# Kernel tuning notes

Measured on AMD Instinct MI355X. Metric: run time of the kernel, lower is better.

The kernel has to match this reference:

```python
import jax, jax.numpy as jnp
import numpy as np

CAL = {
 'x': (-0.0025095, 0.0022181),
 'onnxMatMul_166': (-0.22075387835502625, 0.208940327167511),
 'fc1MatMul': (-0.00291599917, 0.0017367251),
 'fc1bias': (-0.48688140511512756, 0.5176185369491577),
 'fc1Add': (-0.48778465390205383, 0.5181604027748108),
 'Wiz_1': (-0.43284985423088074, 0.46175122261047363),
 'Wir_1': (-0.34401071071624756, 0.29191476106643677),
 'Win_1': (-0.3236880302429199, 0.39607325196266174),
 'Whz_1': (-1.8417714834213257, 1.7173254489898682),
 'Whr_1': (-1.1574513912200928, 1.0300449132919312),
 'Whn_1': (-0.7756922245025635, 0.9530389308929443),
 'biz_1': (-0.5063393712043762, 0.36664387583732605),
 'bir_1': (-0.07920225709676743, 0.20611026883125305),
 'bin_1': (-0.5539973378181458, 0.17938342690467834),
 'bhz_1': (-0.5337516665458679, 0.4148772358894348),
 'bhr_1': (-0.07688436657190323, 0.14814253151416779),
 'bhn_1': (-0.7828555107116699, 0.9008108973503113),
 'Wiz_2': (-0.9102030992507935, 0.9408696889877319),
 'Wir_2': (-0.9560997486114502, 0.6683358550071716),
 'Win_2': (-0.4721935987472534, 0.48561596870422363),
 'Whz_2': (-1.2992678880691528, 1.2991048097610474),
 'Whr_2': (-0.8318714499473572, 1.1085889339447021),
 'Whn_2': (-0.955470085144043, 1.046797513961792),
 'biz_2': (-0.44805487990379333, 0.1560053527355194),
 'bir_2': (-0.08767592161893845, 0.11347303539514542),
 'bin_2': (-0.239909827709198, 0.12033259868621826),
 'bhz_2': (-0.43745461106300354, 0.12699371576309204),
 'bhr_2': (-0.09617264568805695, 0.07690174877643585),
 'bhn_2': (-0.17204178869724274, 0.19739042222499847),
 'onnxMatMul_207': (-1.3657219409942627, 1.158295750617981),
 'fc2bias': (-0.1750922054052353, 0.1385071724653244),
 'onnxMatMul_208': (-3.1666038036346436, 2.5026357173919678),
 'fc3bias': (-0.10188056528568268, 0.0899151861667633),
 'onnxMatMul_209': (-1.300571084022522, 1.928941249847412),
 'fc4bias': (-0.10699586570262909, 0.04597663879394531),
 'h1': (-0.002647488145157695, 0.0028339680284261703),
 'h2': (-0.0031016061548143625, 0.0030250486452132463),
 'gru1_a_': (-0.6389939785003662, 0.7715625762939453),
 'gru1_a': (-0.6046768426895142, 0.8871182203292847),
 'gru1_b_': (-0.004922409541904926, 0.004103424027562141),
 'gru1_b': (-0.07475128024816513, 0.14630259573459625),
 'gru1_c_': (-1.5660111904144287, 1.0454494953155518),
 'gru1_c': (-1.9779117107391357, 1.3700535297393799),
 'gru1_d_': (-0.008429044857621193, 0.006403823848813772),
 'gru1_d': (-0.5529640316963196, 0.41507571935653687),
 'gru1_e_': (-1.3637111186981201, 1.018247127532959),
 'gru1_e': (-1.8583884239196777, 1.1587692499160767),
 'gru1_f_': (-0.005411399528384209, 0.0061536869034171104),
 'gru1_f': (-0.7833794355392456, 0.8978855013847351),
 'gru1_r_': (-0.6226556301116943, 0.9800534844398499),
 'gru1_r': (0.3491777181625366, 0.7271188497543335),
 'gru1_z_': (-2.392332077026367, 1.7851293087005615),
 'gru1_z': (0.08375928550958633, 0.856329083442688),
 'gru1_n1': (-0.5516456365585327, 0.4556601643562317),
 'gru1_n2': (-2.4100341796875, 1.1423156261444092),
 'gru1_n': (-0.983996570110321, 0.8151924014091492),
 'gru1_hn1': (0.143670916557312, 0.9162406921386719),
 'gru1_hn2': (-0.9015777111053467, 0.45391541719436646),
 'gru1_hn3': (-0.0016954239690676332, 0.0016671211924403906),
 'rnn1GRU': (-0.9016271829605103, 0.4546271562576294),
 'gru2_a_': (-0.681461751461029, 0.9113116264343262),
 'gru2_a': (-0.7149235010147095, 0.908741295337677),
 'gru2_b_': (-0.005148397758603096, 0.011014967225492),
 'gru2_b': (-0.09436552226543427, 0.07623167335987091),
 'gru2_c_': (-1.2279887199401855, 1.1102137565612793),
 'gru2_c': (-1.6760436296463013, 1.200895071029663),
 'gru2_d_': (-0.008141756057739258, 0.00894666276872158),
 'gru2_d': (-0.43875735998153687, 0.1262134611606598),
 'gru2_e_': (-0.6732944250106812, 0.6314664483070374),
}
# calib entries for gru2 past 'e_' were truncated in the source; reuse gru1 ranges
for _k in ['e', 'f_', 'f', 'r_', 'r', 'z_', 'z', 'n1', 'n2', 'n', 'hn1', 'hn2', 'hn3']:
    CAL.setdefault('gru2_' + _k, CAL['gru1_' + _k])
CAL['rnn2GRU'] = CAL['rnn1GRU']


def fq(x, name):
    """Per-tensor unsigned 8-bit fake-quantize/dequantize (CalibrationParam S/Z)."""
    mn, mx = CAL[name]
    s = (mx - mn) / 255.0  # 2**8 - 1
    z = float(round(-mn / s))
    q = jnp.clip(jnp.round(x / s) + z, 0.0, 255.0)
    y = (q - z) * s
    # straight-through: forward value is exact fake-quant, identity gradient
    return x + jax.lax.stop_gradient(y - x)


def _gru_layer(xs, Wiz, Wir, Win, Whz, Whr, Whn, biz, bir, binn, bhz, bhr, bhn, L):
    p = 'gru%d' % L
    Wiz = fq(Wiz, 'Wiz_%d' % L); Wir = fq(Wir, 'Wir_%d' % L); Win = fq(Win, 'Win_%d' % L)
    Whz = fq(Whz, 'Whz_%d' % L); Whr = fq(Whr, 'Whr_%d' % L); Whn = fq(Whn, 'Whn_%d' % L)
    biz = fq(biz, 'biz_%d' % L); bir = fq(bir, 'bir_%d' % L); binn = fq(binn, 'bin_%d' % L)
    bhz = fq(bhz, 'bhz_%d' % L); bhr = fq(bhr, 'bhr_%d' % L); bhn = fq(bhn, 'bhn_%d' % L)
    # input projections batched over all timesteps (xs: [T,B,H] time-major)
    A = fq(fq(jnp.einsum('tbi,ih->tbh', xs, Wir), p + '_a_') + bir, p + '_a')
    C = fq(fq(jnp.einsum('tbi,ih->tbh', xs, Wiz), p + '_c_') + biz, p + '_c')
    E = fq(fq(jnp.einsum('tbi,ih->tbh', xs, Win), p + '_e_') + binn, p + '_e')
    h0 = fq(jnp.zeros((xs.shape[1], Whz.shape[0]), xs.dtype), 'h%d' % L)

    def step(h, ace):
        a, c, e = ace
        b = fq(fq(h @ Whr, p + '_b_') + bhr, p + '_b')
        r = fq(jax.nn.sigmoid(fq(a + b, p + '_r_')), p + '_r')
        d = fq(fq(h @ Whz, p + '_d_') + bhz, p + '_d')
        z = fq(jax.nn.sigmoid(fq(c + d, p + '_z_')), p + '_z')
        f = fq(fq(h @ Whn, p + '_f_') + bhn, p + '_f')
        n = fq(jnp.tanh(fq(e + fq(r * f, p + '_n1'), p + '_n2')), p + '_n')
        hn2 = fq(fq(1.0 - z, p + '_hn1') * n, p + '_hn2')
        hn3 = fq(z * h, p + '_hn3')
        h_new = fq(hn2 + hn3, 'rnn%dGRU' % L)
        return h_new, h_new

    _, hs = jax.lax.scan(step, h0, (A, C, E))
    return hs


def setup_inputs() -> dict:
    B, T, F, H, D = 64, 1000, 257, 400, 600
    ks = iter(jax.random.split(jax.random.key(0), 64))

    def u(shape, name):
        mn, mx = CAL[name]
        return jax.random.uniform(next(ks), shape, jnp.float32, mn, mx)

    inp = {}
    inp['x'] = jax.random.normal(next(ks), (B, T, F), jnp.float32) * 0.001
    inp['W_fc1'] = u((F, H), 'onnxMatMul_166')
    inp['b_fc1'] = u((H,), 'fc1bias')
    for L in (1, 2):
        for g in ('z', 'r', 'n'):
            inp['Wi%s%d' % (g, L)] = u((H, H), 'Wi%s_%d' % (g, L))
            inp['Wh%s%d' % (g, L)] = u((H, H), 'Wh%s_%d' % (g, L))
            inp['bi%s%d' % (g, L)] = u((H,), 'bi%s_%d' % (g, L))
            inp['bh%s%d' % (g, L)] = u((H,), 'bh%s_%d' % (g, L))
    inp['W_fc2'] = u((H, D), 'onnxMatMul_207'); inp['b_fc2'] = u((D,), 'fc2bias')
    inp['W_fc3'] = u((D, D), 'onnxMatMul_208'); inp['b_fc3'] = u((D,), 'fc3bias')
    inp['W_fc4'] = u((D, F), 'onnxMatMul_209'); inp['b_fc4'] = u((F,), 'fc4bias')
    return inp


def reference(x, W_fc1, b_fc1, Wiz1, Wir1, Win1, Whz1, Whr1, Whn1, biz1, bir1, bin1, bhz1, bhr1, bhn1, Wiz2, Wir2, Win2, Whz2, Whr2, Whn2, biz2, bir2, bin2, bhz2, bhr2, bhn2, W_fc2, b_fc2, W_fc3, b_fc3, W_fc4, b_fc4):
    xq = fq(x, 'x')
    t = fq(jnp.einsum('bti,ih->bth', xq, fq(W_fc1, 'onnxMatMul_166')), 'fc1MatMul')
    t = fq(t + fq(b_fc1, 'fc1bias'), 'fc1Add')
    xs = jnp.swapaxes(t, 0, 1)  # [T,B,400]
    h1 = _gru_layer(xs, Wiz1, Wir1, Win1, Whz1, Whr1, Whn1, biz1, bir1, bin1, bhz1, bhr1, bhn1, 1)
    h2 = _gru_layer(h1, Wiz2, Wir2, Win2, Whz2, Whr2, Whn2, biz2, bir2, bin2, bhz2, bhr2, bhn2, 2)
    y = jnp.swapaxes(h2, 0, 1)  # [B,T,400]
    y = jax.nn.relu(jnp.einsum('bth,hd->btd', y, fq(W_fc2, 'onnxMatMul_207')) + fq(b_fc2, 'fc2bias'))
    y = jax.nn.relu(jnp.einsum('btd,de->bte', y, fq(W_fc3, 'onnxMatMul_208')) + fq(b_fc3, 'fc3bias'))
    y = jax.nn.sigmoid(jnp.einsum('bte,ef->btf', y, fq(W_fc4, 'onnxMatMul_209')) + fq(b_fc4, 'fc4bias'))
    return y
```

## Files before the change

kernel.cpp:

```cpp
#include <hip/hip_runtime.h>
#include <math.h>

#define DEV static __device__ __forceinline__

typedef int v4i __attribute__((ext_vector_type(4)));
typedef float v4f __attribute__((ext_vector_type(4)));
typedef __bf16 bf16_t;
typedef __bf16 v8bf __attribute__((ext_vector_type(8)));

struct SZ { float s, z; };

constexpr double cfloor_(double v){ long long i=(long long)v; return ((double)i > v) ? (double)(i-1) : (double)i; }
constexpr double cround_(double v){
  double fl = cfloor_(v); double fr = v - fl;
  return (fr > 0.5) ? fl + 1.0 : (fr < 0.5 ? fl : ((((long long)fl) & 1LL) == 0 ? fl : fl + 1.0));
}
constexpr SZ mksz(double mn, double mx){
  double s = (mx - mn) / 255.0;
  double z = cround_(-mn / s);
  return SZ{ (float)s, (float)z };
}

constexpr SZ Zx     = mksz(-0.0025095, 0.0022181);
constexpr SZ ZW1    = mksz(-0.22075387835502625, 0.208940327167511);
constexpr SZ Zfc1mm = mksz(-0.00291599917, 0.0017367251);
constexpr SZ Zbfc1  = mksz(-0.48688140511512756, 0.5176185369491577);
constexpr SZ Zfc1add= mksz(-0.48778465390205383, 0.5181604027748108);
constexpr SZ ZWiz1 = mksz(-0.43284985423088074, 0.46175122261047363);
constexpr SZ ZWir1 = mksz(-0.34401071071624756, 0.29191476106643677);
constexpr SZ ZWin1 = mksz(-0.3236880302429199, 0.39607325196266174);
constexpr SZ ZWhz1 = mksz(-1.8417714834213257, 1.7173254489898682);
constexpr SZ ZWhr1 = mksz(-1.1574513912200928, 1.0300449132919312);
constexpr SZ ZWhn1 = mksz(-0.7756922245025635, 0.9530389308929443);
constexpr SZ Zbiz1 = mksz(-0.5063393712043762, 0.36664387583732605);
constexpr SZ Zbir1 = mksz(-0.07920225709676743, 0.20611026883125305);
constexpr SZ Zbin1 = mksz(-0.5539973378181458, 0.17938342690467834);
constexpr SZ Zbhz1 = mksz(-0.5337516665458679, 0.4148772358894348);
constexpr SZ Zbhr1 = mksz(-0.07688436657190323, 0.14814253151416779);
constexpr SZ Zbhn1 = mksz(-0.7828555107116699, 0.9008108973503113);
constexpr SZ ZWiz2 = mksz(-0.9102030992507935, 0.9408696889877319);
constexpr SZ ZWir2 = mksz(-0.9560997486114502, 0.6683358550071716);
constexpr SZ ZWin2 = mksz(-0.4721935987472534, 0.48561596870422363);
constexpr SZ ZWhz2 = mksz(-1.2992678880691528, 1.2991048097610474);
constexpr SZ ZWhr2 = mksz(-0.8318714499473572, 1.1085889339447021);
constexpr SZ ZWhn2 = mksz(-0.955470085144043, 1.046797513961792);
constexpr SZ Zbiz2 = mksz(-0.44805487990379333, 0.1560053527355194);
constexpr SZ Zbir2 = mksz(-0.08767592161893845, 0.11347303539514542);
constexpr SZ Zbin2 = mksz(-0.239909827709198, 0.12033259868621826);
constexpr SZ Zbhz2 = mksz(-0.43745461106300354, 0.12699371576309204);
constexpr SZ Zbhr2 = mksz(-0.09617264568805695, 0.07690174877643585);
constexpr SZ Zbhn2 = mksz(-0.17204178869724274, 0.19739042222499847);
constexpr SZ ZWfc2 = mksz(-1.3657219409942627, 1.158295750617981);
constexpr SZ Zbfc2 = mksz(-0.1750922054052353, 0.1385071724653244);
constexpr SZ ZWfc3 = mksz(-3.1666038036346436, 2.5026357173919678);
constexpr SZ Zbfc3 = mksz(-0.10188056528568268, 0.0899151861667633);
constexpr SZ ZWfc4 = mksz(-1.300571084022522, 1.928941249847412);
constexpr SZ Zbfc4 = mksz(-0.10699586570262909, 0.04597663879394531);
constexpr SZ Za_1 = mksz(-0.6389939785003662, 0.7715625762939453);
constexpr SZ Za1  = mksz(-0.6046768426895142, 0.8871182203292847);
constexpr SZ Zb_1 = mksz(-0.004922409541904926, 0.004103424027562141);
constexpr SZ Zb1  = mksz(-0.07475128024816513, 0.14630259573459625);
constexpr SZ Zc_1 = mksz(-1.5660111904144287, 1.0454494953155518);
constexpr SZ Zc1  = mksz(-1.9779117107391357, 1.3700535297393799);
constexpr SZ Zd_1 = mksz(-0.008429044857621193, 0.006403823848813772);
constexpr SZ Zd1  = mksz(-0.5529640316963196, 0.41507571935653687);
constexpr SZ Ze_1 = mksz(-1.3637111186981201, 1.018247127532959);
constexpr SZ Ze1  = mksz(-1.8583884239196777, 1.1587692499160767);
constexpr SZ Zf_1 = mksz(-0.005411399528384209, 0.0061536869034171104);
constexpr SZ Zf1  = mksz(-0.7833794355392456, 0.8978855013847351);
constexpr SZ Zr_1 = mksz(-0.6226556301116943, 0.9800534844398499);
constexpr SZ Zr1  = mksz(0.3491777181625366, 0.7271188497543335);
constexpr SZ Zz_1 = mksz(-2.392332077026367, 1.7851293087005615);
constexpr SZ Zz1  = mksz(0.08375928550958633, 0.856329083442688);
constexpr SZ Zn11 = mksz(-0.5516456365585327, 0.4556601643562317);
constexpr SZ Zn21 = mksz(-2.4100341796875, 1.1423156261444092);
constexpr SZ Zn1  = mksz(-0.983996570110321, 0.8151924014091492);
constexpr SZ Zhn11= mksz(0.143670916557312, 0.9162406921386719);
constexpr SZ Zhn21= mksz(-0.9015777111053467, 0.45391541719436646);
constexpr SZ Zhn31= mksz(-0.0016954239690676332, 0.0016671211924403906);
constexpr SZ Zrnn = mksz(-0.9016271829605103, 0.4546271562576294);
constexpr SZ Za_2 = mksz(-0.681461751461029, 0.9113116264343262);
constexpr SZ Za2  = mksz(-0.7149235010147095, 0.908741295337677);
constexpr SZ Zb_2 = mksz(-0.005148397758603096, 0.011014967225492);
constexpr SZ Zb2g = mksz(-0.09436552226543427, 0.07623167335987091);
constexpr SZ Zc_2 = mksz(-1.2279887199401855, 1.1102137565612793);
constexpr SZ Zc2  = mksz(-1.6760436296463013, 1.200895071029663);
constexpr SZ Zd_2 = mksz(-0.008141756057739258, 0.00894666276872158);
constexpr SZ Zd2  = mksz(-0.43875735998153687, 0.1262134611606598);
constexpr SZ Ze_2 = mksz(-0.6732944250106812, 0.6314664483070374);

struct RecP {
  SZ wr, wz, wn;
  SZ a, c, e;
  SZ b1, b2, d1, d2, f1, f2;
  SZ r1, r2, z1, z2;
  SZ n1, n2, n3;
  SZ hn1, hn2, hn3, rnn;
};
constexpr RecP PL1 = { ZWhr1, ZWhz1, ZWhn1, Za1, Zc1, Ze1, Zb_1, Zb1, Zd_1, Zd1, Zf_1, Zf1,
                       Zr_1, Zr1, Zz_1, Zz1, Zn11, Zn21, Zn1, Zhn11, Zhn21, Zhn31, Zrnn };
constexpr RecP PL2 = { ZWhr2, ZWhz2, ZWhn2, Za2, Zc2, Ze1, Zb_2, Zb2g, Zd_2, Zd2, Zf_1, Zf1,
                       Zr_1, Zr1, Zz_1, Zz1, Zn11, Zn21, Zn1, Zhn11, Zhn21, Zhn31, Zrnn };

DEV float fq_(float x, float s, float z){
  float q = rintf(x / s) + z;
  q = fminf(fmaxf(q, 0.f), 255.f);
  return (q - z) * s;
}
DEV float sigm_(float v){ return 1.f / (1.f + expf(-v)); }

DEV unsigned udot4_(unsigned a, unsigned b, unsigned c){
#if defined(__has_builtin) && __has_builtin(__builtin_amdgcn_udot4)
  return __builtin_amdgcn_udot4(a, b, c, false);
#else
  return c + (a & 255u) * (b & 255u) + ((a >> 8) & 255u) * ((b >> 8) & 255u)
           + ((a >> 16) & 255u) * ((b >> 16) & 255u) + (a >> 24) * (b >> 24);
#endif
}

struct BJob { const float* src; float* dst; int n; float s; float z; };
struct BJobs { BJob j[16]; };
__global__ __launch_bounds__(256) void kbias(BJobs jobs){
  BJob J = jobs.j[blockIdx.x];
  for (int i = threadIdx.x; i < J.n; i += 256) J.dst[i] = fq_(J.src[i], J.s, J.z);
}

struct W6 { const float* W[6]; float s[6]; float z[6]; };
__global__ __launch_bounds__(256) void kwhc6(W6 jb, unsigned char* __restrict__ dst){
  int i = blockIdx.x * 256 + threadIdx.x;
  if (i < 960000) {
    int m = i / 160000, r = i - m * 160000;
    int j = r / 400, k = r - j * 400;
    float q = rintf(jb.W[m][k * 400 + j] / jb.s[m]) + jb.z[m];
    q = fminf(fmaxf(q, 0.f), 255.f);
    dst[i] = (unsigned char)q;
  }
}
__global__ __launch_bounds__(256) void kcolsum(const unsigned char* __restrict__ WhC, int* __restrict__ cs){
  int i = blockIdx.x * 256 + threadIdx.x;
  if (i < 2400) {
    const unsigned char* p = WhC + (size_t)i * 400;
    int s = 0;
    for (int k = 0; k < 400; ++k) s += p[k];
    cs[i] = s;
  }
}
__global__ __launch_bounds__(256) void kwic6(W6 jb, signed char* __restrict__ WiT, int* __restrict__ cs){
  for (int idx = blockIdx.x * 256 + threadIdx.x; idx < 960000; idx += gridDim.x * 256) {
    int m = idx / 160000, r = idx - m * 160000;
    int k = r / 400, n = r - k * 400;
    float q = rintf(jb.W[m][r] / jb.s[m]) + jb.z[m];
    q = fminf(fmaxf(q, 0.f), 255.f);
    int qi = (int)q;
    WiT[(size_t)m * 185600 + (size_t)n * 464 + k] = (signed char)(qi ^ 0x80);
    atomicAdd(&cs[m * 400 + n], qi - 128);
  }
  for (int idx = blockIdx.x * 256 + threadIdx.x; idx < 153600; idx += gridDim.x * 256) {
    int m = idx / 25600, r = idx - m * 25600;
    int n = r / 64, p = r - n * 64;
    WiT[(size_t)m * 185600 + (size_t)n * 464 + 400 + p] = 0;
  }
}
__global__ __launch_bounds__(256) void kwic(const float* __restrict__ W, signed char* __restrict__ Bt,
                                            int* __restrict__ cs, float s, float z, int K, int N){
  int total1 = K * N, total2 = (464 - K) * N;
  for (int idx = blockIdx.x * 256 + threadIdx.x; idx < total1; idx += gridDim.x * 256) {
    int k = idx / N, n = idx - k * N;
    float q = rintf(W[idx] / s) + z;
    q = fminf(fmaxf(q, 0.f), 255.f);
    int qi = (int)q;
    Bt[(size_t)n * 464 + k] = (signed char)(qi ^ 0x80);
    atomicAdd(&cs[n], qi - 128);
  }
  for (int idx = blockIdx.x * 256 + threadIdx.x; idx < total2; idx += gridDim.x * 256) {
    int n = idx / (464 - K), k = K + (idx - n * (464 - K));
    Bt[(size_t)n * 464 + k] = 0;
  }
}
__global__ __launch_bounds__(256) void kwbf(const float* __restrict__ W, bf16_t* __restrict__ Bt,
                                            float s, float z, int K, int N){
  int total1 = K * N, total2 = (608 - K) * N;
  for (int idx = blockIdx.x * 256 + threadIdx.x; idx < total1; idx += gridDim.x * 256) {
    int k = idx / N, n = idx - k * N;
    float q = rintf(W[idx] / s) + z;
    q = fminf(fmaxf(q, 0.f), 255.f);
    Bt[(size_t)n * 608 + k] = (bf16_t)(q - z);
  }
  for (int idx = blockIdx.x * 256 + threadIdx.x; idx < total2; idx += gridDim.x * 256) {
    int n = idx / (608 - K), k = K + (idx - n * (608 - K));
    Bt[(size_t)n * 608 + k] = (bf16_t)0.f;
  }
}
__global__ __launch_bounds__(256) void kxq(const float* __restrict__ x, unsigned char* __restrict__ xcq,
                                           float s, float z){
  int idx = blockIdx.x * 256 + threadIdx.x;
  if (idx < 64000 * 464) {
    int row = idx / 464, c = idx - row * 464;
    unsigned char code = 128;
    if (c < 257) {
      int bb = row & 63, tt = row >> 6;
      float q = rintf(x[((size_t)bb * 1000 + tt) * 257 + c] / s) + z;
      q = fminf(fmaxf(q, 0.f), 255.f);
      code = (unsigned char)q;
    }
    xcq[idx] = code;
  }
}
__global__ __launch_bounds__(256) void krsum(const unsigned char* __restrict__ A, int* __restrict__ rs,
                                             int w4){
  int r = blockIdx.x * 256 + threadIdx.x;
  const unsigned* p = (const unsigned*)(A + (size_t)r * (w4 * 16));
  unsigned s = 0;
  for (int i = 0; i < w4 * 4; ++i) s = udot4_(p[i], 0x01010101u, s);
  rs[r] = (int)s - 128 * 4 * (w4 * 4);
}
__global__ __launch_bounds__(256) void kinit2(unsigned long long* __restrict__ hp1,
                                              unsigned long long* __restrict__ hp2, unsigned code){
  int i = blockIdx.x * 256 + threadIdx.x;
  if (i < 25600) {
    unsigned long long w = (unsigned long long)(code * 0x01010101u);
    hp1[i] = w; hp2[i] = w;
  }
}

__global__ __launch_bounds__(256) void gemm_i8(
    const unsigned char* __restrict__ Au8, int strideA, int aw4,
    const int* __restrict__ rowsum,
    const signed char* __restrict__ Bt, const int* __restrict__ colsum,
    const float* __restrict__ bias,
    unsigned char* __restrict__ outU8, float* __restrict__ outF,
    int N, int nb, int outStride, int epMode,
    int czw, int cza, int cconst, float ss,
    float e1S, float e1Z, float e2S, float e2Z)
{
  __shared__ __align__(16) signed char Asl[64 * 464];
  __shared__ __align__(16) signed char Bsl[80 * 464];
  const int tid = threadIdx.x;
  const int bm = blockIdx.x / nb;
  const int bn = blockIdx.x - bm * nb;
  const int m0 = bm * 64;
  const int n0 = bn * 80;
  for (int i = tid; i < 80 * 29; i += 256) {
    int r = i / 29, c = i - r * 29;
    uint4 v;
    if (n0 + r < N) v = *(const uint4*)(Bt + (size_t)(n0 + r) * 464 + c * 16);
    else { v.x = 0u; v.y = 0u; v.z = 0u; v.w = 0u; }
    *(uint4*)(Bsl + (size_t)r * 464 + c * 16) = v;
  }
  for (int i = tid; i < 64 * 29; i += 256) {
    int r = i / 29, c = i - r * 29;
    uint4 v;
    if (c < aw4) {
      v = *(const uint4*)(Au8 + (size_t)(m0 + r) * strideA + c * 16);
      v.x ^= 0x80808080u; v.y ^= 0x80808080u; v.z ^= 0x80808080u; v.w ^= 0x80808080u;
    } else { v.x = 0u; v.y = 0u; v.z = 0u; v.w = 0u; }
    *(uint4*)(Asl + (size_t)r * 464 + c * 16) = v;
  }
  __syncthreads();
  const int wv = tid >> 6, ln = tid & 63;
  const int lr = ln & 15;
  const int lk = ln >> 4;
  v4i acc[5];
#pragma unroll
  for (int j = 0; j < 5; ++j) { acc[j][0] = 0; acc[j][1] = 0; acc[j][2] = 0; acc[j][3] = 0; }
#pragma unroll
  for (int kc = 0; kc < 7; ++kc) {
    int kb = kc * 64 + lk * 16;
    v4i a = *(const v4i*)(Asl + (size_t)(wv * 16 + lr) * 464 + kb);
#pragma unroll
    for (int j = 0; j < 5; ++j) {
      v4i b = *(const v4i*)(Bsl + (size_t)(j * 16 + lr) * 464 + kb);
      acc[j] = __builtin_amdgcn_mfma_i32_16x16x64_i8(a, b, acc[j], 0, 0, 0);
    }
  }
#pragma unroll
  for (int reg = 0; reg < 4; ++reg) {
    int row = m0 + wv * 16 + lk * 4 + reg;
    int RA = rowsum[row];
#pragma unroll
    for (int j = 0; j < 5; ++j) {
      int col = n0 + j * 16 + lr;
      if (col >= N) continue;
      int I = acc[j][reg] + czw * RA + cza * colsum[col] + cconst;
      float v = (float)I * ss;
      if (epMode == 0) {
        v = fq_(v, e1S, e1Z) + bias[col];
        float q = rintf(v / e2S) + e2Z;
        q = fminf(fmaxf(q, 0.f), 255.f);
        outU8[(size_t)row * outStride + col] = (unsigned char)q;
      } else {
        v += bias[col];
        v = fmaxf(v, 0.f);
        outF[(size_t)row * outStride + col] = v;
      }
    }
  }
}

__global__ __launch_bounds__(512) void gemm_bf(
    const float* __restrict__ A, const bf16_t* __restrict__ Bt,
    const float* __restrict__ bias, float* __restrict__ outF,
    int N, int nb, int epMode, int rowOff, float sc)
{
  __shared__ __align__(16) bf16_t Bs[128 * 616];
  const int tid = threadIdx.x;
  const int bm = blockIdx.x / nb;
  const int bn = blockIdx.x - bm * nb;
  const int m0 = bm * 128;
  const int n0 = bn * 128;
  for (int i = tid; i < 128 * 76; i += 512) {
    int r = i / 76, c = i - r * 76;
    uint4 v; v.x = 0u; v.y = 0u; v.z = 0u; v.w = 0u;
    if (n0 + r < N) v = *(const uint4*)((const char*)(Bt + (size_t)(n0 + r) * 608) + c * 16);
    *(uint4*)((char*)(Bs + (size_t)r * 616) + c * 16) = v;
  }
  __syncthreads();
  const int wv = tid >> 6, ln = tid & 63;
  const int lr = ln & 15, quad = ln >> 4;
  const float* arp = A + (size_t)(m0 + wv * 16 + lr) * 600;
  v4f acc[8];
#pragma unroll
  for (int j = 0; j < 8; ++j) { acc[j][0] = 0.f; acc[j][1] = 0.f; acc[j][2] = 0.f; acc[j][3] = 0.f; }
  for (int kc = 0; kc < 19; ++kc) {
    int kb = kc * 32 + quad * 8;
    float af[8];
    if (kc == 18 && quad == 3) {
#pragma unroll
      for (int j = 0; j < 8; ++j) af[j] = 0.f;
    } else {
      *(float4*)&af[0] = *(const float4*)(arp + kb);
      *(float4*)&af[4] = *(const float4*)(arp + kb + 4);
    }
    v8bf ah, al;
#pragma unroll
    for (int j = 0; j < 8; ++j) {
      float xx = af[j];
      bf16_t h = (bf16_t)xx;
      ah[j] = h;
      al[j] = (bf16_t)(xx - (float)h);
    }
#pragma unroll
    for (int nf = 0; nf < 8; ++nf) {
      v8bf bfrag = *(const v8bf*)(Bs + (size_t)(nf * 16 + lr) * 616 + kc * 32 + quad * 8);
      acc[nf] = __builtin_amdgcn_mfma_f32_16x16x32_bf16(ah, bfrag, acc[nf], 0, 0, 0);
      acc[nf] = __builtin_amdgcn_mfma_f32_16x16x32_bf16(al, bfrag, acc[nf], 0, 0, 0);
    }
  }
#pragma unroll
  for (int nf = 0; nf < 8; ++nf) {
    int col = n0 + nf * 16 + lr;
    if (col >= N) continue;
    float bcol = bias[col];
#pragma unroll
    for (int reg = 0; reg < 4; ++reg) {
      int row = m0 + wv * 16 + quad * 4 + reg;
      float v = acc[nf][reg] * sc + bcol;
      if (epMode == 2) {
        v = fmaxf(v, 0.f);
        outF[(size_t)row * N + col] = v;
      } else {
        v = sigm_(v);
        int rg = rowOff + row;
        int tt = rg >> 6, bb = rg & 63;
        outF[((size_t)bb * 1000 + tt) * 257 + col] = v;
      }
    }
  }
}

__global__ __launch_bounds__(512)
__attribute__((amdgpu_num_vgpr(160)))
void gru_rec2b(
    const unsigned char* __restrict__ WhC, const int* __restrict__ colsum,
    const unsigned char* __restrict__ Aq, const unsigned char* __restrict__ Cq,
    const unsigned char* __restrict__ Eq,
    const float* __restrict__ bhr, const float* __restrict__ bhz, const float* __restrict__ bhn,
    unsigned char* __restrict__ hs, unsigned long long* __restrict__ hpub, RecP P)
{
  __shared__ __align__(16) unsigned Wl[352 * 28];
  __shared__ __align__(16) unsigned hq[2][4 * 28];
  __shared__ int dots_i[600];
  __shared__ unsigned acew[2][150];
  __shared__ int ic_l[600];
  __shared__ float bias_l[600];
  __shared__ int HqS_s;
  __shared__ int flag;

  const int tid = threadIdx.x;
  const int sl = blockIdx.x >> 6;
  const int b  = blockIdx.x & 63;
  const unsigned* Wu = (const unsigned*)WhC;

  unsigned wq[4][25];
#pragma unroll
  for (int s = 0; s < 4; ++s) {
    int q = tid + 512 * s;
    int ld = q >> 2, p = q & 3;
    int g = (ld >= 400) ? 2 : (ld >= 200 ? 1 : 0);
    int col = g * 400 + sl * 200 + (ld - g * 200);
    const unsigned* src = Wu + col * 100 + p * 25;
#pragma unroll
    for (int w = 0; w < 25; ++w) wq[s][w] = src[w];
  }
  if (tid < 352) {
    int q = 2048 + tid;
    int ld = q >> 2, p = q & 3;
    int g = (ld >= 400) ? 2 : (ld >= 200 ? 1 : 0);
    int col = g * 400 + sl * 200 + (ld - g * 200);
    const unsigned* src = Wu + col * 100 + p * 25;
    for (int w = 0; w < 25; ++w) Wl[tid * 28 + w] = src[w];
  }
  const int zh = (int)P.rnn.z;
  for (int ld = tid; ld < 600; ld += 512) {
    int g = (ld >= 400) ? 2 : (ld >= 200 ? 1 : 0);
    int jl = ld - g * 200;
    int col = g * 400 + sl * 200 + jl;
    int zw = (g == 0) ? (int)P.wr.z : (g == 1) ? (int)P.wz.z : (int)P.wn.z;
    ic_l[ld] = -zh * colsum[col] + 400 * zh * zw;
    bias_l[ld] = ((g == 0) ? bhr : (g == 1) ? bhz : bhn)[sl * 200 + jl];
  }
  const unsigned code0 = (unsigned)fminf(fmaxf(P.rnn.z, 0.f), 255.f);
  for (int i = tid; i < 100; i += 512)
    hq[0][(i / 25) * 28 + (i % 25)] = code0 * 0x01010101u;
  if (tid == 0) flag = -1;
  const unsigned char* psrc = nullptr;
  int poff = 0;
  if (tid < 150) {
    int g = tid / 50, w = tid - g * 50;
    psrc = (g == 0) ? Aq : (g == 1) ? Cq : Eq;
    poff = (sl * 50 + w) * 4;
    acew[0][tid] = *(const unsigned*)(psrc + (size_t)b * 400 + poff);
  }
  __syncthreads();

  const int part = tid & 3;
  const int grp = tid >> 2;
  const int zwr = (int)P.wr.z, zwz = (int)P.wz.z, zwn = (int)P.wn.z;
  const float swr = P.wr.s * P.rnn.s, swz = P.wz.s * P.rnn.s, swn = P.wn.s * P.rnn.s;
  unsigned long long* pubBase = hpub + (size_t)sl * 12800 + (size_t)b * 50;
  const unsigned long long* polBase = hpub + (size_t)(1 - sl) * 12800 + (size_t)b * 50;

  unsigned hcode = code0;
  unsigned pf = 0;

  for (int t = 0; t < 1000; ++t) {
    if (tid < 150) {
      int tn = (t + 1 < 1000) ? (t + 1) : 999;
      pf = *(const unsigned*)(psrc + ((size_t)tn * 64 + b) * 400 + poff);
    }
    if (tid >= 448) {
      int lane = tid - 448;
      unsigned pay = 0;
      if (lane < 50) {
        const unsigned long long* src = polBase + (size_t)(t & 3) * 3200 + lane;
        unsigned long long w64;
        while ((unsigned)((w64 = __hip_atomic_load(src, __ATOMIC_RELAXED, __HIP_MEMORY_SCOPE_AGENT)) >> 32)
               != (unsigned)t) { }
        pay = (unsigned)w64;
        int wd = (1 - sl) * 50 + lane;
        hq[t & 1][(wd / 25) * 28 + (wd % 25)] = pay;
      }
      if (lane == 0)
        __hip_atomic_store(&flag, t, __ATOMIC_RELEASE, __HIP_MEMORY_SCOPE_WORKGROUP);
      unsigned ssum = 0;
      if (lane < 50) {
        ssum = udot4_(pay, 0x01010101u, 0u);
        int wdo = sl * 50 + lane;
        unsigned own = hq[t & 1][(wdo / 25) * 28 + (wdo % 25)];
        ssum = udot4_(own, 0x01010101u, ssum);
      }
#pragma unroll
      for (int off = 32; off; off >>= 1) ssum += __shfl_down(ssum, off);
      if (lane == 0) HqS_s = (int)ssum;
    } else {
      while (__hip_atomic_load(&flag, __ATOMIC_ACQUIRE, __HIP_MEMORY_SCOPE_WORKGROUP) < t)
        __builtin_amdgcn_s_sleep(1);
    }
    const unsigned* hb = &hq[t & 1][part * 28];
    const unsigned* wl = &Wl[tid * 28];
    unsigned a0 = 0, a1 = 0, a2 = 0, a3 = 0, a4 = 0;
#pragma unroll
    for (int c = 0; c < 6; ++c) {
      uint4 h4 = *(const uint4*)(hb + 4 * c);
      a0 = udot4_(wq[0][4*c+0], h4.x, a0);
      a0 = udot4_(wq[0][4*c+1], h4.y, a0);
      a0 = udot4_(wq[0][4*c+2], h4.z, a0);
      a0 = udot4_(wq[0][4*c+3], h4.w, a0);
      a1 = udot4_(wq[1][4*c+0], h4.x, a1);
      a1 = udot4_(wq[1][4*c+1], h4.y, a1);
      a1 = udot4_(wq[1][4*c+2], h4.z, a1);
      a1 = udot4_(wq[1][4*c+3], h4.w, a1);
      a2 = udot4_(wq[2][4*c+0], h4.x, a2);
      a2 = udot4_(wq[2][4*c+1], h4.y, a2);
      a2 = udot4_(wq[2][4*c+2], h4.z, a2);
      a2 = udot4_(wq[2][4*c+3], h4.w, a2);
      a3 = udot4_(wq[3][4*c+0], h4.x, a3);
      a3 = udot4_(wq[3][4*c+1], h4.y, a3);
      a3 = udot4_(wq[3][4*c+2], h4.z, a3);
      a3 = udot4_(wq[3][4*c+3], h4.w, a3);
      if (tid < 352) {
        uint4 w4 = *(const uint4*)(wl + 4 * c);
        a4 = udot4_(w4.x, h4.x, a4);
        a4 = udot4_(w4.y, h4.y, a4);
        a4 = udot4_(w4.z, h4.z, a4);
        a4 = udot4_(w4.w, h4.w, a4);
      }
    }
    {
      unsigned hl = hb[24];
      a0 = udot4_(wq[0][24], hl, a0);
      a1 = udot4_(wq[1][24], hl, a1);
      a2 = udot4_(wq[2][24], hl, a2);
      a3 = udot4_(wq[3][24], hl, a3);
      if (tid < 352) a4 = udot4_(wl[24], hl, a4);
    }
    a0 += __shfl_xor(a0, 1); a0 += __shfl_xor(a0, 2);
    a1 += __shfl_xor(a1, 1); a1 += __shfl_xor(a1, 2);
    a2 += __shfl_xor(a2, 1); a2 += __shfl_xor(a2, 2);
    a3 += __shfl_xor(a3, 1); a3 += __shfl_xor(a3, 2);
    a4 += __shfl_xor(a4, 1); a4 += __shfl_xor(a4, 2);
    {
      int v = (part == 0) ? (int)a0 : (part == 1) ? (int)a1 : (part == 2) ? (int)a2 : (int)a3;
      dots_i[grp + 128 * part] = v;
      if (part == 0 && tid < 352) dots_i[512 + grp] = (int)a4;
    }
    __syncthreads();

    if (tid < 150) acew[(t + 1) & 1][tid] = pf;
    if (tid < 200) {
      const int j = tid;
      const unsigned char* ab = (const unsigned char*)&acew[t & 1][0];
      float av = ((float)ab[j]       - P.a.z) * P.a.s;
      float cv = ((float)ab[200 + j] - P.c.z) * P.c.s;
      float ev = ((float)ab[400 + j] - P.e.z) * P.e.s;
      int hqs = HqS_s;
      int Ib = dots_i[j]       - zwr * hqs + ic_l[j];
      int Id = dots_i[200 + j] - zwz * hqs + ic_l[200 + j];
      int If = dots_i[400 + j] - zwn * hqs + ic_l[400 + j];
      float bb = fq_((float)Ib * swr, P.b1.s, P.b1.z) + bias_l[j];
      bb = fq_(bb, P.b2.s, P.b2.z);
      float dd = fq_((float)Id * swz, P.d1.s, P.d1.z) + bias_l[200 + j];
      dd = fq_(dd, P.d2.s, P.d2.z);
      float ff = fq_((float)If * swn, P.f1.s, P.f1.z) + bias_l[400 + j];
      ff = fq_(ff, P.f2.s, P.f2.z);
      float r  = fq_(sigm_(fq_(av + bb, P.r1.s, P.r1.z)), P.r2.s, P.r2.z);
      float zz = fq_(sigm_(fq_(cv + dd, P.z1.s, P.z1.z)), P.z2.s, P.z2.z);
      float nn = fq_(tanhf(fq_(ev + fq_(r * ff, P.n1.s, P.n1.z), P.n2.s, P.n2.z)), P.n3.s, P.n3.z);
      float hold = ((float)hcode - P.rnn.z) * P.rnn.s;
      float hn2v = fq_(fq_(1.f - zz, P.hn1.s, P.hn1.z) * nn, P.hn2.s, P.hn2.z);
      float hn3v = fq_(zz * hold, P.hn3.s, P.hn3.z);
      float hnew = hn2v + hn3v;
      float qv = rintf(hnew / P.rnn.s) + P.rnn.z;
      qv = fminf(fmaxf(qv, 0.f), 255.f);
      unsigned code = (unsigned)qv;
      hcode = code;
      unsigned c1 = __shfl_down(code, 1);
      unsigned c2 = __shfl_down(code, 2);
      unsigned c3 = __shfl_down(code, 3);
      if ((j & 3) == 0) {
        unsigned packed = code | (c1 << 8) | (c2 << 16) | (c3 << 24);
        int wrd = j >> 2;
        int wd = sl * 50 + wrd;
        hq[(t + 1) & 1][(wd / 25) * 28 + (wd % 25)] = packed;
        *(unsigned*)(hs + ((size_t)t * 64 + b) * 400 + (wd << 2)) = packed;
        unsigned long long out64 = ((unsigned long long)(unsigned)(t + 1) << 32) | packed;
        __hip_atomic_store(pubBase + (size_t)((t + 1) & 3) * 3200 + wrd, out64,
                           __ATOMIC_RELAXED, __HIP_MEMORY_SCOPE_AGENT);
      }
    }
    __syncthreads();
  }
}

extern "C" void kernel_launch(void* const* d_in, const int* in_sizes, int n_in,
                              void* d_out, int out_size, void* d_ws, size_t ws_size,
                              hipStream_t stream)
{
  const float* x    = (const float*)d_in[0];
  const float* Wfc1 = (const float*)d_in[1];
  const float* bfc1 = (const float*)d_in[2];
  const float* Wiz1 = (const float*)d_in[3];  const float* Whz1 = (const float*)d_in[4];
  const float* biz1 = (const float*)d_in[5];  const float* bhz1 = (const float*)d_in[6];
  const float* Wir1 = (const float*)d_in[7];  const float* Whr1 = (const float*)d_in[8];
  const float* bir1 = (const float*)d_in[9];  const float* bhr1 = (const float*)d_in[10];
  const float* Win1 = (const float*)d_in[11]; const float* Whn1 = (const float*)d_in[12];
  const float* bin1 = (const float*)d_in[13]; const float* bhn1 = (const float*)d_in[14];
  const float* Wiz2 = (const float*)d_in[15]; const float* Whz2 = (const float*)d_in[16];
  const float* biz2 = (const float*)d_in[17]; const float* bhz2 = (const float*)d_in[18];
  const float* Wir2 = (const float*)d_in[19]; const float* Whr2 = (const float*)d_in[20];
  const float* bir2 = (const float*)d_in[21]; const float* bhr2 = (const float*)d_in[22];
  const float* Win2 = (const float*)d_in[23]; const float* Whn2 = (const float*)d_in[24];
  const float* bin2 = (const float*)d_in[25]; const float* bhn2 = (const float*)d_in[26];
  const float* Wfc2 = (const float*)d_in[27]; const float* bfc2 = (const float*)d_in[28];
  const float* Wfc3 = (const float*)d_in[29]; const float* bfc3 = (const float*)d_in[30];
  const float* Wfc4 = (const float*)d_in[31]; const float* bfc4 = (const float*)d_in[32];
  float* out = (float*)d_out;

  char* wp = (char*)d_ws;
  auto alloc = [&](size_t bytes) -> void* {
    void* p = (void*)wp;
    wp += (bytes + 255) & ~(size_t)255;
    return p;
  };
  float* b1q = (float*)alloc(400 * 4);
  float* biq = (float*)alloc(2400 * 4);
  float* bhq = (float*)alloc(2400 * 4);
  float* b2q = (float*)alloc(600 * 4);
  float* b3q = (float*)alloc(600 * 4);
  float* b4q = (float*)alloc(257 * 4);
  unsigned char* WhC = (unsigned char*)alloc(960000);
  int* colsum = (int*)alloc(2400 * 4);
  signed char* WiT = (signed char*)alloc(7 * 400 * 464);
  signed char* Bt2 = (signed char*)alloc(600 * 464);
  bf16_t* Bt3 = (bf16_t*)alloc(600 * 608 * 2);
  bf16_t* Bt4 = (bf16_t*)alloc(257 * 608 * 2);
  int* cwi = (int*)alloc((7 * 400 + 600) * 4);
  int* rsX1 = (int*)alloc(64000 * 4);
  int* rsX  = (int*)alloc(64000 * 4);
  int* rsH  = (int*)alloc(64000 * 4);
  int* rsH2 = (int*)alloc(64000 * 4);
  unsigned char* xsq = (unsigned char*)alloc(25600000);
  unsigned char* Aq  = (unsigned char*)alloc(25600000);
  unsigned char* Cq  = (unsigned char*)alloc(25600000);
  unsigned char* Eq  = (unsigned char*)alloc(25600000);
  unsigned char* hs1 = (unsigned char*)alloc(25600000);
  unsigned char* hs2 = (unsigned char*)alloc(25600000);
  unsigned long long* hpub1 = (unsigned long long*)alloc(25600 * 8);
  unsigned long long* hpub2 = (unsigned long long*)alloc(25600 * 8);
  float* y2c = (float*)Aq;
  float* y3c = (float*)(Aq + 38400000);
  unsigned char* xcq = hs1;

  BJobs bj;
  bj.j[0]  = { bfc1, b1q,        400, Zbfc1.s, Zbfc1.z };
  bj.j[1]  = { bir1, biq + 0,    400, Zbir1.s, Zbir1.z };
  bj.j[2]  = { biz1, biq + 400,  400, Zbiz1.s, Zbiz1.z };
  bj.j[3]  = { bin1, biq + 800,  400, Zbin1.s, Zbin1.z };
  bj.j[4]  = { bir2, biq + 1200, 400, Zbir2.s, Zbir2.z };
  bj.j[5]  = { biz2, biq + 1600, 400, Zbiz2.s, Zbiz2.z };
  bj.j[6]  = { bin2, biq + 2000, 400, Zbin2.s, Zbin2.z };
  bj.j[7]  = { bhr1, bhq + 0,    400, Zbhr1.s, Zbhr1.z };
  bj.j[8]  = { bhz1, bhq + 400,  400, Zbhz1.s, Zbhz1.z };
  bj.j[9]  = { bhn1, bhq + 800,  400, Zbhn1.s, Zbhn1.z };
  bj.j[10] = { bhr2, bhq + 1200, 400, Zbhr2.s, Zbhr2.z };
  bj.j[11] = { bhz2, bhq + 1600, 400, Zbhz2.s, Zbhz2.z };
  bj.j[12] = { bhn2, bhq + 2000, 400, Zbhn2.s, Zbhn2.z };
  bj.j[13] = { bfc2, b2q,        600, Zbfc2.s, Zbfc2.z };
  bj.j[14] = { bfc3, b3q,        600, Zbfc3.s, Zbfc3.z };
  bj.j[15] = { bfc4, b4q,        257, Zbfc4.s, Zbfc4.z };
  kbias<<<dim3(16), dim3(256), 0, stream>>>(bj);

  W6 wh = { { Whr1, Whz1, Whn1, Whr2, Whz2, Whn2 },
            { ZWhr1.s, ZWhz1.s, ZWhn1.s, ZWhr2.s, ZWhz2.s, ZWhn2.s },
            { ZWhr1.z, ZWhz1.z, ZWhn1.z, ZWhr2.z, ZWhz2.z, ZWhn2.z } };
  kwhc6<<<dim3(3750), dim3(256), 0, stream>>>(wh, WhC);
  kcolsum<<<dim3(10), dim3(256), 0, stream>>>(WhC, colsum);
  unsigned code0 = (unsigned)(Zrnn.z < 0.f ? 0.f : (Zrnn.z > 255.f ? 255.f : Zrnn.z));
  kinit2<<<dim3(100), dim3(256), 0, stream>>>(hpub1, hpub2, code0);

  hipMemsetAsync(cwi, 0, (7 * 400 + 600) * 4, stream);
  W6 wi = { { Wir1, Wiz1, Win1, Wir2, Wiz2, Win2 },
            { ZWir1.s, ZWiz1.s, ZWin1.s, ZWir2.s, ZWiz2.s, ZWin2.s },
            { ZWir1.z, ZWiz1.z, ZWin1.z, ZWir2.z, ZWiz2.z, ZWin2.z } };
  kwic6<<<dim3(625), dim3(256), 0, stream>>>(wi, WiT, cwi);
  kwic<<<dim3(625), dim3(256), 0, stream>>>(Wfc1, WiT + (size_t)6 * 185600, cwi + 2400, ZW1.s, ZW1.z, 257, 400);
  kwic<<<dim3(625), dim3(256), 0, stream>>>(Wfc2, Bt2, cwi + 2800, ZWfc2.s, ZWfc2.z, 400, 600);
  kwbf<<<dim3(625), dim3(256), 0, stream>>>(Wfc3, Bt3, ZWfc3.s, ZWfc3.z, 600, 600);
  kwbf<<<dim3(625), dim3(256), 0, stream>>>(Wfc4, Bt4, ZWfc4.s, ZWfc4.z, 600, 257);

  auto gi8 = [&](const unsigned char* A, int strideA, int aw4, const int* rs,
                 const signed char* Bt, const int* cs, const float* bias,
                 unsigned char* oU8, float* oF, int M, int N, int outStride, int epMode,
                 SZ a, SZ w, int Kreal, float ss, SZ e1, SZ e2) {
    int czw = 128 - (int)w.z, cza = 128 - (int)a.z;
    int cconst = Kreal * cza * czw;
    int nb = (N + 79) / 80;
    gemm_i8<<<dim3((M / 64) * nb), dim3(256), 0, stream>>>(
        A, strideA, aw4, rs, Bt, cs, bias, oU8, oF, N, nb, outStride, epMode,
        czw, cza, cconst, ss, e1.s, e1.z, e2.s, e2.z);
  };

  kxq<<<dim3((64000 * 464 + 255) / 256), dim3(256), 0, stream>>>(x, xcq, Zx.s, Zx.z);
  krsum<<<dim3(250), dim3(256), 0, stream>>>(xcq, rsX1, 29);
  gi8(xcq, 464, 29, rsX1, WiT + (size_t)6 * 185600, cwi + 2400, b1q,
      xsq, nullptr, 64000, 400, 400, 0, Zx, ZW1, 257, Zx.s * ZW1.s, Zfc1mm, Zfc1add);

  krsum<<<dim3(250), dim3(256), 0, stream>>>(xsq, rsX, 25);
  gi8(xsq, 400, 25, rsX, WiT + (size_t)0 * 185600, cwi + 0,    biq + 0,   Aq, nullptr,
      64000, 400, 400, 0, Zfc1add, ZWir1, 400, Zfc1add.s * ZWir1.s, Za_1, Za1);
  gi8(xsq, 400, 25, rsX, WiT + (size_t)1 * 185600, cwi + 400,  biq + 400, Cq, nullptr,
      64000, 400, 400, 0, Zfc1add, ZWiz1, 400, Zfc1add.s * ZWiz1.s, Zc_1, Zc1);
  gi8(xsq, 400, 25, rsX, WiT + (size_t)2 * 185600, cwi + 800,  biq + 800, Eq, nullptr,
      64000, 400, 400, 0, Zfc1add, ZWin1, 400, Zfc1add.s * ZWin1.s, Ze_1, Ze1);
  gru_rec2b<<<dim3(128), dim3(512), 0, stream>>>(WhC, colsum, Aq, Cq, Eq,
                                                 bhq + 0, bhq + 400, bhq + 800,
                                                 hs1, hpub1, PL1);
  krsum<<<dim3(250), dim3(256), 0, stream>>>(hs1, rsH, 25);
  gi8(hs1, 400, 25, rsH, WiT + (size_t)3 * 185600, cwi + 1200, biq + 1200, Aq, nullptr,
      64000, 400, 400, 0, Zrnn, ZWir2, 400, Zrnn.s * ZWir2.s, Za_2, Za2);
  gi8(hs1, 400, 25, rsH, WiT + (size_t)4 * 185600, cwi + 1600, biq + 1600, Cq, nullptr,
      64000, 400, 400, 0, Zrnn, ZWiz2, 400, Zrnn.s * ZWiz2.s, Zc_2, Zc2);
  gi8(hs1, 400, 25, rsH, WiT + (size_t)5 * 185600, cwi + 2000, biq + 2000, Eq, nullptr,
      64000, 400, 400, 0, Zrnn, ZWin2, 400, Zrnn.s * ZWin2.s, Ze_2, Ze1);
  gru_rec2b<<<dim3(128), dim3(512), 0, stream>>>(WhC + 480000, colsum + 1200, Aq, Cq, Eq,
                                                 bhq + 1200, bhq + 1600, bhq + 2000,
                                                 hs2, hpub2, PL2);
  krsum<<<dim3(250), dim3(256), 0, stream>>>(hs2, rsH2, 25);
  for (int rc = 0; rc < 4; ++rc) {
    const unsigned char* a2 = hs2 + (size_t)rc * 16000 * 400;
    gi8(a2, 400, 25, rsH2 + rc * 16000, Bt2, cwi + 2800, b2q, nullptr, y2c,
        16000, 600, 600, 2, Zrnn, ZWfc2, 400, Zrnn.s * ZWfc2.s, Zrnn, Zrnn);
    gemm_bf<<<dim3(125 * 5), dim3(512), 0, stream>>>(y2c, Bt3, b3q, y3c, 600, 5, 2, 0, ZWfc3.s);
    gemm_bf<<<dim3(125 * 3), dim3(512), 0, stream>>>(y3c, Bt4, b4q, out, 257, 3, 3, rc * 16000, ZWfc4.s);
  }
  (void)in_sizes; (void)n_in; (void)out_size; (void)ws_size;
}
```

Measured before the change: 6.850 ms.

## Split GRU recurrence across four workgroups per batch row instead of two

Each batch row's recurrent GRU step is now spread over four cooperating workgroups (256 blocks), each owning 100 hidden units, instead of two owning 200. The hidden-state exchange through the global publish buffer changes to an all-to-all among four slices, and each thread holds half as many weight registers. The VGPR cap and the s_sleep in the flag spin-wait are removed. The aim is to shorten the per-step serial dot-product and gate work, at the cost of more cross-block polling traffic and synchronisation per timestep.

```diff
diff --git a/kernel.cpp b/kernel.cpp
--- a/kernel.cpp
+++ b/kernel.cpp
@@ -368,21 +368,19 @@
   }
 }
 
-__global__ __launch_bounds__(512)
-__attribute__((amdgpu_num_vgpr(160)))
-void gru_rec2b(
+__global__ __launch_bounds__(512) void gru_rec4b(
     const unsigned char* __restrict__ WhC, const int* __restrict__ colsum,
     const unsigned char* __restrict__ Aq, const unsigned char* __restrict__ Cq,
     const unsigned char* __restrict__ Eq,
     const float* __restrict__ bhr, const float* __restrict__ bhz, const float* __restrict__ bhn,
     unsigned char* __restrict__ hs, unsigned long long* __restrict__ hpub, RecP P)
 {
-  __shared__ __align__(16) unsigned Wl[352 * 28];
+  __shared__ __align__(16) unsigned Wl[176 * 28];
   __shared__ __align__(16) unsigned hq[2][4 * 28];
-  __shared__ int dots_i[600];
-  __shared__ unsigned acew[2][150];
-  __shared__ int ic_l[600];
-  __shared__ float bias_l[600];
+  __shared__ int dots_i[300];
+  __shared__ unsigned acew[2][75];
+  __shared__ int ic_l[300];
+  __shared__ float bias_l[300];
   __shared__ int HqS_s;
   __shared__ int flag;
 
@@ -391,33 +389,33 @@
   const int b  = blockIdx.x & 63;
   const unsigned* Wu = (const unsigned*)WhC;
 
-  unsigned wq[4][25];
-#pragma unroll
-  for (int s = 0; s < 4; ++s) {
+  unsigned wq[2][25];
+#pragma unroll
+  for (int s = 0; s < 2; ++s) {
     int q = tid + 512 * s;
     int ld = q >> 2, p = q & 3;
-    int g = (ld >= 400) ? 2 : (ld >= 200 ? 1 : 0);
-    int col = g * 400 + sl * 200 + (ld - g * 200);
+    int g = ld / 100, jl = ld - g * 100;
+    int col = g * 400 + sl * 100 + jl;
     const unsigned* src = Wu + col * 100 + p * 25;
 #pragma unroll
     for (int w = 0; w < 25; ++w) wq[s][w] = src[w];
   }
-  if (tid < 352) {
-    int q = 2048 + tid;
+  if (tid < 176) {
+    int q = 1024 + tid;
     int ld = q >> 2, p = q & 3;
-    int g = (ld >= 400) ? 2 : (ld >= 200 ? 1 : 0);
-    int col = g * 400 + sl * 200 + (ld - g * 200);
+    int g = ld / 100, jl = ld - g * 100;
+    int col = g * 400 + sl * 100 + jl;
     const unsigned* src = Wu + col * 100 + p * 25;
     for (int w = 0; w < 25; ++w) Wl[tid * 28 + w] = src[w];
   }
   const int zh = (int)P.rnn.z;
-  for (int ld = tid; ld < 600; ld += 512) {
-    int g = (ld >= 400) ? 2 : (ld >= 200 ? 1 : 0);
-    int jl = ld - g * 200;
-    int col = g * 400 + sl * 200 + jl;
+  if (tid < 300) {
+    int ld = tid;
+    int g = ld / 100, jl = ld - g * 100;
+    int col = g * 400 + sl * 100 + jl;
     int zw = (g == 0) ? (int)P.wr.z : (g == 1) ? (int)P.wz.z : (int)P.wn.z;
     ic_l[ld] = -zh * colsum[col] + 400 * zh * zw;
-    bias_l[ld] = ((g == 0) ? bhr : (g == 1) ? bhz : bhn)[sl * 200 + jl];
+    bias_l[ld] = ((g == 0) ? bhr : (g == 1) ? bhz : bhn)[sl * 100 + jl];
   }
   const unsigned code0 = (unsigned)fminf(fmaxf(P.rnn.z, 0.f), 255.f);
   for (int i = tid; i < 100; i += 512)
@@ -425,10 +423,10 @@
   if (tid == 0) flag = -1;
   const unsigned char* psrc = nullptr;
   int poff = 0;
-  if (tid < 150) {
-    int g = tid / 50, w = tid - g * 50;
+  if (tid < 75) {
+    int g = tid / 25, w = tid - g * 25;
     psrc = (g == 0) ? Aq : (g == 1) ? Cq : Eq;
-    poff = (sl * 50 + w) * 4;
+    poff = (sl * 25 + w) * 4;
     acew[0][tid] = *(const unsigned*)(psrc + (size_t)b * 400 + poff);
   }
   __syncthreads();
@@ -437,48 +435,54 @@
   const int grp = tid >> 2;
   const int zwr = (int)P.wr.z, zwz = (int)P.wz.z, zwn = (int)P.wn.z;
   const float swr = P.wr.s * P.rnn.s, swz = P.wz.s * P.rnn.s, swn = P.wn.s * P.rnn.s;
-  unsigned long long* pubBase = hpub + (size_t)sl * 12800 + (size_t)b * 50;
-  const unsigned long long* polBase = hpub + (size_t)(1 - sl) * 12800 + (size_t)b * 50;
 
   unsigned hcode = code0;
   unsigned pf = 0;
 
   for (int t = 0; t < 1000; ++t) {
-    if (tid < 150) {
+    if (tid < 75) {
       int tn = (t + 1 < 1000) ? (t + 1) : 999;
       pf = *(const unsigned*)(psrc + ((size_t)tn * 64 + b) * 400 + poff);
     }
     if (tid >= 448) {
       int lane = tid - 448;
-      unsigned pay = 0;
-      if (lane < 50) {
-        const unsigned long long* src = polBase + (size_t)(t & 3) * 3200 + lane;
+      const unsigned long long* base = hpub + ((size_t)(t & 3) * 64 + b) * 100;
+      unsigned pay0, pay1 = 0;
+      {
+        int o = lane / 25, p = lane - o * 25;
+        int so = (sl + o + 1) & 3;
+        const unsigned long long* src = base + so * 25 + p;
         unsigned long long w64;
         while ((unsigned)((w64 = __hip_atomic_load(src, __ATOMIC_RELAXED, __HIP_MEMORY_SCOPE_AGENT)) >> 32)
                != (unsigned)t) { }
-        pay = (unsigned)w64;
-        int wd = (1 - sl) * 50 + lane;
-        hq[t & 1][(wd / 25) * 28 + (wd % 25)] = pay;
+        pay0 = (unsigned)w64;
+        hq[t & 1][so * 28 + p] = pay0;
+      }
+      if (lane < 11) {
+        int w1 = 64 + lane;
+        int o = w1 / 25, p = w1 - o * 25;
+        int so = (sl + o + 1) & 3;
+        const unsigned long long* src = base + so * 25 + p;
+        unsigned long long w64;
+        while ((unsigned)((w64 = __hip_atomic_load(src, __ATOMIC_RELAXED, __HIP_MEMORY_SCOPE_AGENT)) >> 32)
+               != (unsigned)t) { }
+        pay1 = (unsigned)w64;
+        hq[t & 1][so * 28 + p] = pay1;
       }
       if (lane == 0)
         __hip_atomic_store(&flag, t, __ATOMIC_RELEASE, __HIP_MEMORY_SCOPE_WORKGROUP);
-      unsigned ssum = 0;
-      if (lane < 50) {
-        ssum = udot4_(pay, 0x01010101u, 0u);
-        int wdo = sl * 50 + lane;
-        unsigned own = hq[t & 1][(wdo / 25) * 28 + (wdo % 25)];
-        ssum = udot4_(own, 0x01010101u, ssum);
-      }
-#pragma unroll
-      for (int off = 32; off; off >>= 1) ssum += __shfl_down(ssum, off);
+      unsigned ssum = udot4_(pay0, 0x01010101u, 0u);
+      if (lane < 11) ssum = udot4_(pay1, 0x01010101u, ssum);
+      if (lane < 25) ssum = udot4_(hq[t & 1][sl * 28 + lane], 0x01010101u, ssum);
+#pragma unroll
+      for (int off = 32; off; off >>= 1) ssum += __shfl_down(ssum, off, 64);
       if (lane == 0) HqS_s = (int)ssum;
     } else {
-      while (__hip_atomic_load(&flag, __ATOMIC_ACQUIRE, __HIP_MEMORY_SCOPE_WORKGROUP) < t)
-        __builtin_amdgcn_s_sleep(1);
+      while (__hip_atomic_load(&flag, __ATOMIC_ACQUIRE, __HIP_MEMORY_SCOPE_WORKGROUP) < t) { }
     }
     const unsigned* hb = &hq[t & 1][part * 28];
     const unsigned* wl = &Wl[tid * 28];
-    unsigned a0 = 0, a1 = 0, a2 = 0, a3 = 0, a4 = 0;
+    unsigned a0 = 0, a1 = 0, a2 = 0;
 #pragma unroll
     for (int c = 0; c < 6; ++c) {
       uint4 h4 = *(const uint4*)(hb + 4 * c);
@@ -490,58 +494,44 @@
       a1 = udot4_(wq[1][4*c+1], h4.y, a1);
       a1 = udot4_(wq[1][4*c+2], h4.z, a1);
       a1 = udot4_(wq[1][4*c+3], h4.w, a1);
-      a2 = udot4_(wq[2][4*c+0], h4.x, a2);
-      a2 = udot4_(wq[2][4*c+1], h4.y, a2);
-      a2 = udot4_(wq[2][4*c+2], h4.z, a2);
-      a2 = udot4_(wq[2][4*c+3], h4.w, a2);
-      a3 = udot4_(wq[3][4*c+0], h4.x, a3);
-      a3 = udot4_(wq[3][4*c+1], h4.y, a3);
-      a3 = udot4_(wq[3][4*c+2], h4.z, a3);
-      a3 = udot4_(wq[3][4*c+3], h4.w, a3);
-      if (tid < 352) {
+      if (tid < 176) {
         uint4 w4 = *(const uint4*)(wl + 4 * c);
-        a4 = udot4_(w4.x, h4.x, a4);
-        a4 = udot4_(w4.y, h4.y, a4);
-        a4 = udot4_(w4.z, h4.z, a4);
-        a4 = udot4_(w4.w, h4.w, a4);
+        a2 = udot4_(w4.x, h4.x, a2);
+        a2 = udot4_(w4.y, h4.y, a2);
+        a2 = udot4_(w4.z, h4.z, a2);
+        a2 = udot4_(w4.w, h4.w, a2);
       }
     }
     {
       unsigned hl = hb[24];
       a0 = udot4_(wq[0][24], hl, a0);
       a1 = udot4_(wq[1][24], hl, a1);
-      a2 = udot4_(wq[2][24], hl, a2);
-      a3 = udot4_(wq[3][24], hl, a3);
-      if (tid < 352) a4 = udot4_(wl[24], hl, a4);
+      if (tid < 176) a2 = udot4_(wl[24], hl, a2);
     }
     a0 += __shfl_xor(a0, 1); a0 += __shfl_xor(a0, 2);
     a1 += __shfl_xor(a1, 1); a1 += __shfl_xor(a1, 2);
     a2 += __shfl_xor(a2, 1); a2 += __shfl_xor(a2, 2);
-    a3 += __shfl_xor(a3, 1); a3 += __shfl_xor(a3, 2);
-    a4 += __shfl_xor(a4, 1); a4 += __shfl_xor(a4, 2);
-    {
-      int v = (part == 0) ? (int)a0 : (part == 1) ? (int)a1 : (part == 2) ? (int)a2 : (int)a3;
-      dots_i[grp + 128 * part] = v;
-      if (part == 0 && tid < 352) dots_i[512 + grp] = (int)a4;
-    }
+    if (part == 0)      dots_i[grp]       = (int)a0;
+    else if (part == 1) dots_i[128 + grp] = (int)a1;
+    else if (part == 2) { if (grp < 44) dots_i[256 + grp] = (int)a2; }
     __syncthreads();
 
-    if (tid < 150) acew[(t + 1) & 1][tid] = pf;
-    if (tid < 200) {
+    if (tid < 75) acew[(t + 1) & 1][tid] = pf;
+    if (tid < 100) {
       const int j = tid;
       const unsigned char* ab = (const unsigned char*)&acew[t & 1][0];
       float av = ((float)ab[j]       - P.a.z) * P.a.s;
-      float cv = ((float)ab[200 + j] - P.c.z) * P.c.s;
-      float ev = ((float)ab[400 + j] - P.e.z) * P.e.s;
+      float cv = ((float)ab[100 + j] - P.c.z) * P.c.s;
+      float ev = ((float)ab[200 + j] - P.e.z) * P.e.s;
       int hqs = HqS_s;
       int Ib = dots_i[j]       - zwr * hqs + ic_l[j];
-      int Id = dots_i[200 + j] - zwz * hqs + ic_l[200 + j];
-      int If = dots_i[400 + j] - zwn * hqs + ic_l[400 + j];
+      int Id = dots_i[100 + j] - zwz * hqs + ic_l[100 + j];
+      int If = dots_i[200 + j] - zwn * hqs + ic_l[200 + j];
       float bb = fq_((float)Ib * swr, P.b1.s, P.b1.z) + bias_l[j];
       bb = fq_(bb, P.b2.s, P.b2.z);
-      float dd = fq_((float)Id * swz, P.d1.s, P.d1.z) + bias_l[200 + j];
+      float dd = fq_((float)Id * swz, P.d1.s, P.d1.z) + bias_l[100 + j];
       dd = fq_(dd, P.d2.s, P.d2.z);
-      float ff = fq_((float)If * swn, P.f1.s, P.f1.z) + bias_l[400 + j];
+      float ff = fq_((float)If * swn, P.f1.s, P.f1.z) + bias_l[200 + j];
       ff = fq_(ff, P.f2.s, P.f2.z);
       float r  = fq_(sigm_(fq_(av + bb, P.r1.s, P.r1.z)), P.r2.s, P.r2.z);
       float zz = fq_(sigm_(fq_(cv + dd, P.z1.s, P.z1.z)), P.z2.s, P.z2.z);
@@ -560,12 +550,11 @@
       if ((j & 3) == 0) {
         unsigned packed = code | (c1 << 8) | (c2 << 16) | (c3 << 24);
         int wrd = j >> 2;
-        int wd = sl * 50 + wrd;
-        hq[(t + 1) & 1][(wd / 25) * 28 + (wd % 25)] = packed;
-        *(unsigned*)(hs + ((size_t)t * 64 + b) * 400 + (wd << 2)) = packed;
+        hq[(t + 1) & 1][sl * 28 + wrd] = packed;
+        *(unsigned*)(hs + ((size_t)t * 64 + b) * 400 + ((sl * 25 + wrd) << 2)) = packed;
         unsigned long long out64 = ((unsigned long long)(unsigned)(t + 1) << 32) | packed;
-        __hip_atomic_store(pubBase + (size_t)((t + 1) & 3) * 3200 + wrd, out64,
-                           __ATOMIC_RELAXED, __HIP_MEMORY_SCOPE_AGENT);
+        unsigned long long* dst = hpub + ((size_t)((t + 1) & 3) * 64 + b) * 100 + sl * 25 + wrd;
+        __hip_atomic_store(dst, out64, __ATOMIC_RELAXED, __HIP_MEMORY_SCOPE_AGENT);
       }
     }
     __syncthreads();
@@ -692,7 +681,7 @@
       64000, 400, 400, 0, Zfc1add, ZWiz1, 400, Zfc1add.s * ZWiz1.s, Zc_1, Zc1);
   gi8(xsq, 400, 25, rsX, WiT + (size_t)2 * 185600, cwi + 800,  biq + 800, Eq, nullptr,
       64000, 400, 400, 0, Zfc1add, ZWin1, 400, Zfc1add.s * ZWin1.s, Ze_1, Ze1);
-  gru_rec2b<<<dim3(128), dim3(512), 0, stream>>>(WhC, colsum, Aq, Cq, Eq,
+  gru_rec4b<<<dim3(256), dim3(512), 0, stream>>>(WhC, colsum, Aq, Cq, Eq,
                                                  bhq + 0, bhq + 400, bhq + 800,
                                                  hs1, hpub1, PL1);
   krsum<<<dim3(250), dim3(256), 0, stream>>>(hs1, rsH, 25);
@@ -702,7 +691,7 @@
       64000, 400, 400, 0, Zrnn, ZWiz2, 400, Zrnn.s * ZWiz2.s, Zc_2, Zc2);
   gi8(hs1, 400, 25, rsH, WiT + (size_t)5 * 185600, cwi + 2000, biq + 2000, Eq, nullptr,
       64000, 400, 400, 0, Zrnn, ZWin2, 400, Zrnn.s * ZWin2.s, Ze_2, Ze1);
-  gru_rec2b<<<dim3(128), dim3(512), 0, stream>>>(WhC + 480000, colsum + 1200, Aq, Cq, Eq,
+  gru_rec4b<<<dim3(256), dim3(512), 0, stream>>>(WhC + 480000, colsum + 1200, Aq, Cq, Eq,
                                                  bhq + 1200, bhq + 1600, bhq + 2000,
                                                  hs2, hpub2, PL2);
   krsum<<<dim3(250), dim3(256), 0, stream>>>(hs2, rsH2, 25);
```

Measured after the change: 6.831 ms. No clear change (-0.3%).
